# Optimization experiments

Hardware: AMD Instinct MI355X
Metric: run time of the kernel (lower is better)

## Reference

```python
import jax, jax.numpy as jnp
import numpy as np
from jax import lax

SMOOTH = 1.0
CONVEX = 1.0
MAX_IT = 500  # eval=False path in legendre
TOL = 0.001
B, C, H = 1024, 64, 128


def _icnn(x, Wy0, by0, Wy1, by1, Wz1, Wy2, by2, Wz2):
    # ICNN: softplus chain with positive (clamped) Wz weights, plus strongly-convex quadratic term
    h = jax.nn.softplus(x @ Wy0.T + by0)                                   # [B, H]
    h = jax.nn.softplus(h @ jnp.clip(Wz1, 0.0, 1e10).T + x @ Wy1.T + by1)  # [B, H]
    out = jax.nn.softplus(h @ jnp.clip(Wz2, 0.0, 1e10).T + x @ Wy2.T + by2)  # [B, 1]
    return out + (1.0 / (2.0 * SMOOTH)) * jnp.sum(x * x, axis=1, keepdims=True)


def _legendre(z, Wy0, by0, Wy1, by1, Wz1, Wy2, by2, Wz2):
    # grad of per-sample scalar ICNN output w.r.t. its input (sum trick: outputs are sample-wise independent)
    grad_icnn = jax.grad(lambda xx: jnp.sum(_icnn(xx, Wy0, by0, Wy1, by1, Wz1, Wy2, by2, Wz2)))
    step = 2.0 * SMOOTH

    def body(carry, i):
        x1, done = carry
        g = grad_icnn(x1)
        new_x1 = x1 + (step / (i + 1.0)) * (z - g)
        x1 = jnp.where(done, x1, new_x1)
        err = jnp.mean(jnp.linalg.norm(z - g, axis=1))
        done = jnp.logical_or(done, err < TOL)
        return (x1, done), None

    x1_0 = jnp.ones_like(z)
    (x1, _), _ = lax.scan(body, (x1_0, jnp.array(False)), jnp.arange(MAX_IT, dtype=z.dtype))
    return x1 + CONVEX * z


def _xavier(key, shape):
    fan_out, fan_in = shape
    std = np.sqrt(2.0 / (fan_in + fan_out))
    return jax.random.normal(key, shape, dtype=jnp.float32) * std


def setup_inputs() -> dict:
    key = jax.random.key(0)
    ks = jax.random.split(key, 8)
    bound0 = 1.0 / np.sqrt(C)
    return {
        "x": jax.random.normal(ks[0], (B, C), dtype=jnp.float32),
        "Wy0": _xavier(ks[1], (H, C)),
        "by0": jax.random.uniform(ks[2], (H,), dtype=jnp.float32, minval=-bound0, maxval=bound0),
        "Wy1": _xavier(ks[3], (H, C)),
        "by1": jax.random.uniform(ks[4], (H,), dtype=jnp.float32, minval=-bound0, maxval=bound0),
        "Wz1": _xavier(ks[5], (H, H)),
        "Wy2": _xavier(ks[6], (1, C)),
        "by2": jax.random.uniform(ks[7], (1,), dtype=jnp.float32, minval=-bound0, maxval=bound0),
        "Wz2": _xavier(jax.random.fold_in(key, 99), (1, H)),
    }


def reference(x, Wy0, by0, Wy1, by1, Wz1, Wy2, by2, Wz2):
    return _legendre(x, Wy0, by0, Wy1, by1, Wz1, Wy2, by2, Wz2)
```

## Files before the change

kernel.cpp:

```cpp
#include <hip/hip_runtime.h>
#include <math.h>

#define NB 1024
#define NC 64
#define NH 128
#define MAX_IT 500
#define TOLF 1e-3f

typedef _Float16 f16x8 __attribute__((ext_vector_type(8)));
typedef float    f32x4 __attribute__((ext_vector_type(4)));
typedef _Float16 h2    __attribute__((ext_vector_type(2)));

#define MFMA(a, b, c) __builtin_amdgcn_mfma_f32_16x16x32_f16((a), (b), (c), 0, 0, 0)

__device__ __forceinline__ unsigned pack_h2(float a, float b) {
    union { h2 h; unsigned u; } cv;
    cv.h.x = (_Float16)a; cv.h.y = (_Float16)b; return cv.u;
}
__device__ __forceinline__ float rcp_fast(float x) {
#if __has_builtin(__builtin_amdgcn_rcpf)
    return __builtin_amdgcn_rcpf(x);
#else
    return 1.0f / x;
#endif
}
__device__ __forceinline__ void sigsp(float a, float& sig, float& sp) {
    const float e = __expf(-fabsf(a));
    const float r = rcp_fast(1.0f + e);
    sig = (a >= 0.0f) ? r : e * r;
    sp  = fmaxf(a, 0.0f) + __logf(1.0f + e);
}
__device__ __forceinline__ float sigm(float a) {
    const float e = __expf(-fabsf(a));
    const float r = rcp_fast(1.0f + e);
    return (a >= 0.0f) ? r : e * r;
}
__device__ __forceinline__ float clp(float x) { return fmaxf(x, 0.0f); }

__launch_bounds__(256, 1)
__global__ void blnn_kernel(const float* __restrict__ xin,
                            const float* __restrict__ Wy0,
                            const float* __restrict__ by0,
                            const float* __restrict__ Wy1,
                            const float* __restrict__ by1,
                            const float* __restrict__ Wz1,
                            const float* __restrict__ Wy2,
                            const float* __restrict__ by2,
                            const float* __restrict__ Wz2,
                            float* __restrict__ out)
{
    __shared__ uint4 WA0q[16 * 64];
    __shared__ uint4 WA1q[16 * 64];
    __shared__ uint4 WAZq[32 * 64];
    __shared__ uint4 WZTq[32 * 64];
    __shared__ uint4 W1Tq[16 * 64];
    __shared__ uint4 W0Tq[16 * 64];
    __shared__ __align__(16) _Float16 xact [4 * 72];
    __shared__ __align__(16) _Float16 h0act[4 * 136];
    __shared__ __align__(16) _Float16 v1act[4 * 136];
    __shared__ __align__(16) _Float16 v0act[4 * 136];
    __shared__ __align__(16) float by0f[128], by1f[128], wz2f[128];
    __shared__ __align__(16) float hp[16], pxp[16], npar[16];

    const int tid  = threadIdx.x;
    const int w    = tid >> 6;
    const int l    = tid & 63;
    const int n    = l & 15;
    const int n4   = n & 3;
    const int quad = l >> 4;
    const int blk4 = blockIdx.x * 4;

    for (int f = tid; f < 16 * 64; f += 256) {
        const int tile = f >> 6, q = f & 63;
        const int mt = tile >> 1, ks = tile & 1;
        const int row = mt * 16 + (q & 15);
        const int k0  = ks * 32 + ((q >> 4) << 3);
        const float* p0 = Wy0 + row * 64 + k0;
        WA0q[f] = make_uint4(pack_h2(p0[0], p0[1]), pack_h2(p0[2], p0[3]),
                             pack_h2(p0[4], p0[5]), pack_h2(p0[6], p0[7]));
        const float* p1 = Wy1 + row * 64 + k0;
        WA1q[f] = make_uint4(pack_h2(p1[0], p1[1]), pack_h2(p1[2], p1[3]),
                             pack_h2(p1[4], p1[5]), pack_h2(p1[6], p1[7]));
    }
    for (int f = tid; f < 32 * 64; f += 256) {
        const int tile = f >> 6, q = f & 63;
        const int mt = tile >> 2, ks = tile & 3;
        const int row = mt * 16 + (q & 15);
        const int k0  = ks * 32 + ((q >> 4) << 3);
        const float* p = Wz1 + row * 128 + k0;
        WAZq[f] = make_uint4(pack_h2(clp(p[0]), clp(p[1])), pack_h2(clp(p[2]), clp(p[3])),
                             pack_h2(clp(p[4]), clp(p[5])), pack_h2(clp(p[6]), clp(p[7])));
        const float* pt = Wz1 + k0 * 128 + row;
        WZTq[f] = make_uint4(pack_h2(clp(pt[0]),   clp(pt[128])),
                             pack_h2(clp(pt[256]), clp(pt[384])),
                             pack_h2(clp(pt[512]), clp(pt[640])),
                             pack_h2(clp(pt[768]), clp(pt[896])));
    }
    for (int f = tid; f < 16 * 64; f += 256) {
        const int tile = f >> 6, q = f & 63;
        const int mt = tile >> 2, ks = tile & 3;
        const int rowT = mt * 16 + (q & 15);
        const int k0   = ks * 32 + ((q >> 4) << 3);
        const float* p1 = Wy1 + k0 * 64 + rowT;
        W1Tq[f] = make_uint4(pack_h2(p1[0],   p1[64]),  pack_h2(p1[128], p1[192]),
                             pack_h2(p1[256], p1[320]), pack_h2(p1[384], p1[448]));
        const float* p0 = Wy0 + k0 * 64 + rowT;
        W0Tq[f] = make_uint4(pack_h2(p0[0],   p0[64]),  pack_h2(p0[128], p0[192]),
                             pack_h2(p0[256], p0[320]), pack_h2(p0[384], p0[448]));
    }
    if (tid < 128) {
        by0f[tid] = by0[tid];
        by1f[tid] = by1[tid];
        wz2f[tid] = fmaxf(Wz2[tid], 0.0f);
    }
    {
        const int nn = tid >> 6, cc = tid & 63;
        xact[nn * 72 + cc] = (_Float16)xin[(blk4 + nn) * 64 + cc];
    }

    const float4 z4  = ((const float4*)xin)[(blk4 + n4) * 16 + w * 4 + quad];
    const float4 wy4 = ((const float4*)Wy2)[w * 4 + quad];
    float zr[4]   = {z4.x, z4.y, z4.z, z4.w};
    float wy2r[4] = {wy4.x, wy4.y, wy4.z, wy4.w};
    float xcur[4] = {zr[0], zr[1], zr[2], zr[3]};
    float lamE = 1.0f, prevn2 = 3.4e38f;
    const float b2 = by2[0];

    {
        float pxs = wy2r[0]*xcur[0] + wy2r[1]*xcur[1] + wy2r[2]*xcur[2] + wy2r[3]*xcur[3];
        pxs += __shfl_xor(pxs, 16, 64);
        pxs += __shfl_xor(pxs, 32, 64);
        if (l < 4) pxp[l * 4 + w] = pxs;
    }
    __syncthreads();

    const f16x8* WA0v = (const f16x8*)WA0q;
    const f16x8* WA1v = (const f16x8*)WA1q;
    const f16x8* WAZv = (const f16x8*)WAZq;
    const f16x8* WZTv = (const f16x8*)WZTq;
    const f16x8* W1Tv = (const f16x8*)W1Tq;
    const f16x8* W0Tv = (const f16x8*)W0Tq;
    const float4* by0v = (const float4*)by0f;
    const float4* by1v = (const float4*)by1f;
    const float4* wz2v = (const float4*)wz2f;
    const _Float16* xrow  = xact  + n4 * 72;
    const _Float16* h0row = h0act + n4 * 136;
    const _Float16* v1row = v1act + n4 * 136;
    const _Float16* v0row = v0act + n4 * 136;

    float sig0[2][4];

    for (int it = 0; it < MAX_IT; ++it) {
        f16x8 bx0 = *(const f16x8*)(xrow + quad * 8);
        f16x8 bx1 = *(const f16x8*)(xrow + 32 + quad * 8);
        #pragma unroll
        for (int mi = 0; mi < 2; ++mi) {
            const int mt = w + 4 * mi;
            f32x4 acc = {0.f, 0.f, 0.f, 0.f};
            acc = MFMA(WA0v[(mt * 2 + 0) * 64 + l], bx0, acc);
            acc = MFMA(WA0v[(mt * 2 + 1) * 64 + l], bx1, acc);
            const float4 bb = by0v[mt * 4 + quad];
            float sp0, sp1, sp2, sp3;
            sigsp(acc[0] + bb.x, sig0[mi][0], sp0);
            sigsp(acc[1] + bb.y, sig0[mi][1], sp1);
            sigsp(acc[2] + bb.z, sig0[mi][2], sp2);
            sigsp(acc[3] + bb.w, sig0[mi][3], sp3);
            if (n < 4)
                *(uint2*)&h0act[n4 * 136 + mt * 16 + quad * 4] =
                    make_uint2(pack_h2(sp0, sp1), pack_h2(sp2, sp3));
        }
        __syncthreads();

        f16x8 bh0 = *(const f16x8*)(h0row + quad * 8);
        f16x8 bh1 = *(const f16x8*)(h0row + 32 + quad * 8);
        f16x8 bh2 = *(const f16x8*)(h0row + 64 + quad * 8);
        f16x8 bh3 = *(const f16x8*)(h0row + 96 + quad * 8);
        float hsum = 0.0f;
        #pragma unroll
        for (int mi = 0; mi < 2; ++mi) {
            const int mt = w + 4 * mi;
            f32x4 acc = {0.f, 0.f, 0.f, 0.f};
            acc = MFMA(WAZv[(mt * 4 + 0) * 64 + l], bh0, acc);
            acc = MFMA(WAZv[(mt * 4 + 1) * 64 + l], bh1, acc);
            acc = MFMA(WAZv[(mt * 4 + 2) * 64 + l], bh2, acc);
            acc = MFMA(WAZv[(mt * 4 + 3) * 64 + l], bh3, acc);
            acc = MFMA(WA1v[(mt * 2 + 0) * 64 + l], bx0, acc);
            acc = MFMA(WA1v[(mt * 2 + 1) * 64 + l], bx1, acc);
            const float4 bb  = by1v[mt * 4 + quad];
            const float4 wzq = wz2v[mt * 4 + quad];
            float s1, h1;
            sigsp(acc[0] + bb.x, s1, h1); hsum = fmaf(wzq.x, h1, hsum);
            const float t0 = s1 * wzq.x;
            sigsp(acc[1] + bb.y, s1, h1); hsum = fmaf(wzq.y, h1, hsum);
            const float t1 = s1 * wzq.y;
            sigsp(acc[2] + bb.z, s1, h1); hsum = fmaf(wzq.z, h1, hsum);
            const float t2 = s1 * wzq.z;
            sigsp(acc[3] + bb.w, s1, h1); hsum = fmaf(wzq.w, h1, hsum);
            const float t3 = s1 * wzq.w;
            if (n < 4)
                *(uint2*)&v1act[n4 * 136 + mt * 16 + quad * 4] =
                    make_uint2(pack_h2(t0, t1), pack_h2(t2, t3));
        }
        hsum += __shfl_xor(hsum, 16, 64);
        hsum += __shfl_xor(hsum, 32, 64);
        if (l < 4) hp[l * 4 + w] = hsum;
        __syncthreads();

        float sg2c;
        {
            const float4 hv = ((const float4*)hp)[n4];
            const float4 pv = ((const float4*)pxp)[n4];
            sg2c = sigm(hv.x + hv.y + hv.z + hv.w + pv.x + pv.y + pv.z + pv.w + b2);
        }
        f16x8 bv10 = *(const f16x8*)(v1row + quad * 8);
        f16x8 bv11 = *(const f16x8*)(v1row + 32 + quad * 8);
        f16x8 bv12 = *(const f16x8*)(v1row + 64 + quad * 8);
        f16x8 bv13 = *(const f16x8*)(v1row + 96 + quad * 8);
        #pragma unroll
        for (int mi = 0; mi < 2; ++mi) {
            const int mt = w + 4 * mi;
            f32x4 acc = {0.f, 0.f, 0.f, 0.f};
            acc = MFMA(WZTv[(mt * 4 + 0) * 64 + l], bv10, acc);
            acc = MFMA(WZTv[(mt * 4 + 1) * 64 + l], bv11, acc);
            acc = MFMA(WZTv[(mt * 4 + 2) * 64 + l], bv12, acc);
            acc = MFMA(WZTv[(mt * 4 + 3) * 64 + l], bv13, acc);
            const float a0 = sig0[mi][0] * sg2c * acc[0];
            const float a1 = sig0[mi][1] * sg2c * acc[1];
            const float a2 = sig0[mi][2] * sg2c * acc[2];
            const float a3 = sig0[mi][3] * sg2c * acc[3];
            if (n < 4)
                *(uint2*)&v0act[n4 * 136 + mt * 16 + quad * 4] =
                    make_uint2(pack_h2(a0, a1), pack_h2(a2, a3));
        }
        f32x4 accg = {0.f, 0.f, 0.f, 0.f};
        accg = MFMA(W1Tv[(w * 4 + 0) * 64 + l], bv10, accg);
        accg = MFMA(W1Tv[(w * 4 + 1) * 64 + l], bv11, accg);
        accg = MFMA(W1Tv[(w * 4 + 2) * 64 + l], bv12, accg);
        accg = MFMA(W1Tv[(w * 4 + 3) * 64 + l], bv13, accg);
        __syncthreads();

        f16x8 bv00 = *(const f16x8*)(v0row + quad * 8);
        f16x8 bv01 = *(const f16x8*)(v0row + 32 + quad * 8);
        f16x8 bv02 = *(const f16x8*)(v0row + 64 + quad * 8);
        f16x8 bv03 = *(const f16x8*)(v0row + 96 + quad * 8);
        f32x4 acc0 = {0.f, 0.f, 0.f, 0.f};
        acc0 = MFMA(W0Tv[(w * 4 + 0) * 64 + l], bv00, acc0);
        acc0 = MFMA(W0Tv[(w * 4 + 1) * 64 + l], bv01, acc0);
        acc0 = MFMA(W0Tv[(w * 4 + 2) * 64 + l], bv02, acc0);
        acc0 = MFMA(W0Tv[(w * 4 + 3) * 64 + l], bv03, acc0);
        float resid[4];
        float r2 = 0.0f;
        #pragma unroll
        for (int r = 0; r < 4; ++r) {
            const float g = xcur[r] + sg2c * wy2r[r] + sg2c * accg[r] + acc0[r];
            resid[r] = zr[r] - g;
            r2 = fmaf(resid[r], resid[r], r2);
        }
        r2 += __shfl_xor(r2, 16, 64);
        r2 += __shfl_xor(r2, 32, 64);
        if (l < 4) npar[l * 4 + w] = r2;
        __syncthreads();

        const float4 q0 = ((const float4*)npar)[0];
        const float4 q1 = ((const float4*)npar)[1];
        const float4 q2 = ((const float4*)npar)[2];
        const float4 q3 = ((const float4*)npar)[3];
        const float s0 = q0.x + q0.y + q0.z + q0.w;
        const float s1 = q1.x + q1.y + q1.z + q1.w;
        const float s2 = q2.x + q2.y + q2.z + q2.w;
        const float s3 = q3.x + q3.y + q3.z + q3.w;
        const float T2 = TOLF * TOLF;
        if (s0 < T2 && s1 < T2 && s2 < T2 && s3 < T2) break;

        const float myn2 = (n4 == 0) ? s0 : (n4 == 1) ? s1 : (n4 == 2) ? s2 : s3;
        if (myn2 >= T2) {
            if (myn2 > prevn2 * 0.998f)      lamE *= 0.5f;
            else if (myn2 < 0.81f * prevn2)  lamE = fminf(lamE * 1.15f, 1.0f);
            const float step = fmaxf(lamE, 1.0f / (float)(it + 2));
            #pragma unroll
            for (int r = 0; r < 4; ++r) xcur[r] = fmaf(step, resid[r], xcur[r]);
            prevn2 = myn2;
        }
        {
            float pxs = wy2r[0]*xcur[0] + wy2r[1]*xcur[1] + wy2r[2]*xcur[2] + wy2r[3]*xcur[3];
            pxs += __shfl_xor(pxs, 16, 64);
            pxs += __shfl_xor(pxs, 32, 64);
            if (l < 4) pxp[l * 4 + w] = pxs;
        }
        if (n < 4)
            *(uint2*)&xact[n4 * 72 + w * 16 + quad * 4] =
                make_uint2(pack_h2(xcur[0], xcur[1]), pack_h2(xcur[2], xcur[3]));
        __syncthreads();
    }

    if (n < 4) {
        float4 o;
        o.x = xcur[0] + zr[0]; o.y = xcur[1] + zr[1];
        o.z = xcur[2] + zr[2]; o.w = xcur[3] + zr[3];
        ((float4*)out)[(blk4 + n4) * 16 + w * 4 + quad] = o;
    }
}

extern "C" void kernel_launch(void* const* d_in, const int* in_sizes, int n_in,
                              void* d_out, int out_size, void* d_ws, size_t ws_size,
                              hipStream_t stream) {
    const float* xin = (const float*)d_in[0];
    const float* Wy0 = (const float*)d_in[1];
    const float* by0 = (const float*)d_in[2];
    const float* Wy1 = (const float*)d_in[3];
    const float* by1 = (const float*)d_in[4];
    const float* Wz1 = (const float*)d_in[5];
    const float* Wy2 = (const float*)d_in[6];
    const float* by2 = (const float*)d_in[7];
    const float* Wz2 = (const float*)d_in[8];
    float* out = (float*)d_out;

    blnn_kernel<<<dim3(NB / 4), dim3(256), 0, stream>>>(
        xin, Wy0, by0, Wy1, by1, Wz1, Wy2, by2, Wz2, out);
}
```

Measured before the change: 88.29 us.

## Halve samples per block, hold adjoint weights in registers, prepack via separate kernel

Each block now handles 2 samples instead of 4, so the grid doubles to 512 blocks and launch bounds allow 2 blocks per CU. The transposed weights used in the backward pass (Wz1^T, Wy1^T, Wy0^T) are packed to fp16 once by a new pre-kernel into workspace and then loaded into registers instead of LDS, which cuts LDS use and per-iteration LDS reads. The step-size rule also drops the increase branch for lamE, which changes the convergence behaviour and possibly the iteration count. Register pressure goes up, and with only 2 samples per 16-column MFMA tile most of the tensor-core work is wasted padding.

```diff
diff --git a/kernel.cpp b/kernel.cpp
--- a/kernel.cpp
+++ b/kernel.cpp
@@ -2,8 +2,6 @@
 #include <math.h>
 
 #define NB 1024
-#define NC 64
-#define NH 128
 #define MAX_IT 500
 #define TOLF 1e-3f
 
@@ -16,6 +14,9 @@
 __device__ __forceinline__ unsigned pack_h2(float a, float b) {
     union { h2 h; unsigned u; } cv;
     cv.h.x = (_Float16)a; cv.h.y = (_Float16)b; return cv.u;
+}
+__device__ __forceinline__ f16x8 as_f16x8(uint4 u) {
+    union { uint4 u; f16x8 h; } cv; cv.u = u; return cv.h;
 }
 __device__ __forceinline__ float rcp_fast(float x) {
 #if __has_builtin(__builtin_amdgcn_rcpf)
@@ -37,7 +38,44 @@
 }
 __device__ __forceinline__ float clp(float x) { return fmaxf(x, 0.0f); }
 
-__launch_bounds__(256, 1)
+__global__ void pack_adj(const float* __restrict__ Wy0,
+                         const float* __restrict__ Wy1,
+                         const float* __restrict__ Wz1,
+                         uint4* __restrict__ ws)
+{
+    const int f = blockIdx.x * 256 + threadIdx.x;
+    if (f < 2048) {
+        const int tile = f >> 6, q = f & 63;
+        const int mt = tile >> 2, ks = tile & 3;
+        const int row = mt * 16 + (q & 15);
+        const int k0  = ks * 32 + ((q >> 4) << 3);
+        const float* pt = Wz1 + k0 * 128 + row;
+        ws[f] = make_uint4(pack_h2(clp(pt[0]),   clp(pt[128])),
+                           pack_h2(clp(pt[256]), clp(pt[384])),
+                           pack_h2(clp(pt[512]), clp(pt[640])),
+                           pack_h2(clp(pt[768]), clp(pt[896])));
+    } else if (f < 3072) {
+        const int f2 = f - 2048;
+        const int tile = f2 >> 6, q = f2 & 63;
+        const int mt = tile >> 2, ks = tile & 3;
+        const int rowT = mt * 16 + (q & 15);
+        const int k0   = ks * 32 + ((q >> 4) << 3);
+        const float* p = Wy1 + k0 * 64 + rowT;
+        ws[f] = make_uint4(pack_h2(p[0],   p[64]),  pack_h2(p[128], p[192]),
+                           pack_h2(p[256], p[320]), pack_h2(p[384], p[448]));
+    } else {
+        const int f2 = f - 3072;
+        const int tile = f2 >> 6, q = f2 & 63;
+        const int mt = tile >> 2, ks = tile & 3;
+        const int rowT = mt * 16 + (q & 15);
+        const int k0   = ks * 32 + ((q >> 4) << 3);
+        const float* p = Wy0 + k0 * 64 + rowT;
+        ws[f] = make_uint4(pack_h2(p[0],   p[64]),  pack_h2(p[128], p[192]),
+                           pack_h2(p[256], p[320]), pack_h2(p[384], p[448]));
+    }
+}
+
+__launch_bounds__(256, 2)
 __global__ void blnn_kernel(const float* __restrict__ xin,
                             const float* __restrict__ Wy0,
                             const float* __restrict__ by0,
@@ -47,28 +85,26 @@
                             const float* __restrict__ Wy2,
                             const float* __restrict__ by2,
                             const float* __restrict__ Wz2,
+                            const uint4* __restrict__ adjw,
                             float* __restrict__ out)
 {
     __shared__ uint4 WA0q[16 * 64];
     __shared__ uint4 WA1q[16 * 64];
     __shared__ uint4 WAZq[32 * 64];
-    __shared__ uint4 WZTq[32 * 64];
-    __shared__ uint4 W1Tq[16 * 64];
-    __shared__ uint4 W0Tq[16 * 64];
-    __shared__ __align__(16) _Float16 xact [4 * 72];
-    __shared__ __align__(16) _Float16 h0act[4 * 136];
-    __shared__ __align__(16) _Float16 v1act[4 * 136];
-    __shared__ __align__(16) _Float16 v0act[4 * 136];
+    __shared__ __align__(16) _Float16 xact [2 * 72];
+    __shared__ __align__(16) _Float16 h0act[2 * 136];
+    __shared__ __align__(16) _Float16 v1act[2 * 136];
+    __shared__ __align__(16) _Float16 v0act[2 * 136];
     __shared__ __align__(16) float by0f[128], by1f[128], wz2f[128];
-    __shared__ __align__(16) float hp[16], pxp[16], npar[16];
+    __shared__ __align__(16) float hp[8], pxp[8], npar[8];
 
     const int tid  = threadIdx.x;
     const int w    = tid >> 6;
     const int l    = tid & 63;
     const int n    = l & 15;
-    const int n4   = n & 3;
+    const int n2   = n & 1;
     const int quad = l >> 4;
-    const int blk4 = blockIdx.x * 4;
+    const int blk2 = blockIdx.x * 2;
 
     for (int f = tid; f < 16 * 64; f += 256) {
         const int tile = f >> 6, q = f & 63;
@@ -90,35 +126,38 @@
         const float* p = Wz1 + row * 128 + k0;
         WAZq[f] = make_uint4(pack_h2(clp(p[0]), clp(p[1])), pack_h2(clp(p[2]), clp(p[3])),
                              pack_h2(clp(p[4]), clp(p[5])), pack_h2(clp(p[6]), clp(p[7])));
-        const float* pt = Wz1 + k0 * 128 + row;
-        WZTq[f] = make_uint4(pack_h2(clp(pt[0]),   clp(pt[128])),
-                             pack_h2(clp(pt[256]), clp(pt[384])),
-                             pack_h2(clp(pt[512]), clp(pt[640])),
-                             pack_h2(clp(pt[768]), clp(pt[896])));
-    }
-    for (int f = tid; f < 16 * 64; f += 256) {
-        const int tile = f >> 6, q = f & 63;
-        const int mt = tile >> 2, ks = tile & 3;
-        const int rowT = mt * 16 + (q & 15);
-        const int k0   = ks * 32 + ((q >> 4) << 3);
-        const float* p1 = Wy1 + k0 * 64 + rowT;
-        W1Tq[f] = make_uint4(pack_h2(p1[0],   p1[64]),  pack_h2(p1[128], p1[192]),
-                             pack_h2(p1[256], p1[320]), pack_h2(p1[384], p1[448]));
-        const float* p0 = Wy0 + k0 * 64 + rowT;
-        W0Tq[f] = make_uint4(pack_h2(p0[0],   p0[64]),  pack_h2(p0[128], p0[192]),
-                             pack_h2(p0[256], p0[320]), pack_h2(p0[384], p0[448]));
     }
     if (tid < 128) {
         by0f[tid] = by0[tid];
         by1f[tid] = by1[tid];
         wz2f[tid] = fmaxf(Wz2[tid], 0.0f);
     }
-    {
+    if (tid < 128) {
         const int nn = tid >> 6, cc = tid & 63;
-        xact[nn * 72 + cc] = (_Float16)xin[(blk4 + nn) * 64 + cc];
-    }
-
-    const float4 z4  = ((const float4*)xin)[(blk4 + n4) * 16 + w * 4 + quad];
+        xact[nn * 72 + cc] = (_Float16)xin[(blk2 + nn) * 64 + cc];
+    }
+
+    const uint4* WZTg = adjw;
+    const uint4* W1Tg = adjw + 2048;
+    const uint4* W0Tg = adjw + 3072;
+    const uint4 rz0 = WZTg[((w    ) * 4 + 0) * 64 + l];
+    const uint4 rz1 = WZTg[((w    ) * 4 + 1) * 64 + l];
+    const uint4 rz2 = WZTg[((w    ) * 4 + 2) * 64 + l];
+    const uint4 rz3 = WZTg[((w    ) * 4 + 3) * 64 + l];
+    const uint4 rz4 = WZTg[((w + 4) * 4 + 0) * 64 + l];
+    const uint4 rz5 = WZTg[((w + 4) * 4 + 1) * 64 + l];
+    const uint4 rz6 = WZTg[((w + 4) * 4 + 2) * 64 + l];
+    const uint4 rz7 = WZTg[((w + 4) * 4 + 3) * 64 + l];
+    const uint4 r1_0 = W1Tg[(w * 4 + 0) * 64 + l];
+    const uint4 r1_1 = W1Tg[(w * 4 + 1) * 64 + l];
+    const uint4 r1_2 = W1Tg[(w * 4 + 2) * 64 + l];
+    const uint4 r1_3 = W1Tg[(w * 4 + 3) * 64 + l];
+    const uint4 r0_0 = W0Tg[(w * 4 + 0) * 64 + l];
+    const uint4 r0_1 = W0Tg[(w * 4 + 1) * 64 + l];
+    const uint4 r0_2 = W0Tg[(w * 4 + 2) * 64 + l];
+    const uint4 r0_3 = W0Tg[(w * 4 + 3) * 64 + l];
+
+    const float4 z4  = ((const float4*)xin)[(blk2 + n2) * 16 + w * 4 + quad];
     const float4 wy4 = ((const float4*)Wy2)[w * 4 + quad];
     float zr[4]   = {z4.x, z4.y, z4.z, z4.w};
     float wy2r[4] = {wy4.x, wy4.y, wy4.z, wy4.w};
@@ -130,23 +169,20 @@
         float pxs = wy2r[0]*xcur[0] + wy2r[1]*xcur[1] + wy2r[2]*xcur[2] + wy2r[3]*xcur[3];
         pxs += __shfl_xor(pxs, 16, 64);
         pxs += __shfl_xor(pxs, 32, 64);
-        if (l < 4) pxp[l * 4 + w] = pxs;
+        if (l < 2) pxp[l * 4 + w] = pxs;
     }
     __syncthreads();
 
     const f16x8* WA0v = (const f16x8*)WA0q;
     const f16x8* WA1v = (const f16x8*)WA1q;
     const f16x8* WAZv = (const f16x8*)WAZq;
-    const f16x8* WZTv = (const f16x8*)WZTq;
-    const f16x8* W1Tv = (const f16x8*)W1Tq;
-    const f16x8* W0Tv = (const f16x8*)W0Tq;
     const float4* by0v = (const float4*)by0f;
     const float4* by1v = (const float4*)by1f;
     const float4* wz2v = (const float4*)wz2f;
-    const _Float16* xrow  = xact  + n4 * 72;
-    const _Float16* h0row = h0act + n4 * 136;
-    const _Float16* v1row = v1act + n4 * 136;
-    const _Float16* v0row = v0act + n4 * 136;
+    const _Float16* xrow  = xact  + n2 * 72;
+    const _Float16* h0row = h0act + n2 * 136;
+    const _Float16* v1row = v1act + n2 * 136;
+    const _Float16* v0row = v0act + n2 * 136;
 
     float sig0[2][4];
 
@@ -165,8 +201,8 @@
             sigsp(acc[1] + bb.y, sig0[mi][1], sp1);
             sigsp(acc[2] + bb.z, sig0[mi][2], sp2);
             sigsp(acc[3] + bb.w, sig0[mi][3], sp3);
-            if (n < 4)
-                *(uint2*)&h0act[n4 * 136 + mt * 16 + quad * 4] =
+            if (n < 2)
+                *(uint2*)&h0act[n2 * 136 + mt * 16 + quad * 4] =
                     make_uint2(pack_h2(sp0, sp1), pack_h2(sp2, sp3));
         }
         __syncthreads();
@@ -197,46 +233,58 @@
             const float t2 = s1 * wzq.z;
             sigsp(acc[3] + bb.w, s1, h1); hsum = fmaf(wzq.w, h1, hsum);
             const float t3 = s1 * wzq.w;
-            if (n < 4)
-                *(uint2*)&v1act[n4 * 136 + mt * 16 + quad * 4] =
+            if (n < 2)
+                *(uint2*)&v1act[n2 * 136 + mt * 16 + quad * 4] =
                     make_uint2(pack_h2(t0, t1), pack_h2(t2, t3));
         }
         hsum += __shfl_xor(hsum, 16, 64);
         hsum += __shfl_xor(hsum, 32, 64);
-        if (l < 4) hp[l * 4 + w] = hsum;
+        if (l < 2) hp[l * 4 + w] = hsum;
         __syncthreads();
 
         float sg2c;
         {
-            const float4 hv = ((const float4*)hp)[n4];
-            const float4 pv = ((const float4*)pxp)[n4];
+            const float4 hv = ((const float4*)hp)[n2];
+            const float4 pv = ((const float4*)pxp)[n2];
             sg2c = sigm(hv.x + hv.y + hv.z + hv.w + pv.x + pv.y + pv.z + pv.w + b2);
         }
         f16x8 bv10 = *(const f16x8*)(v1row + quad * 8);
         f16x8 bv11 = *(const f16x8*)(v1row + 32 + quad * 8);
         f16x8 bv12 = *(const f16x8*)(v1row + 64 + quad * 8);
         f16x8 bv13 = *(const f16x8*)(v1row + 96 + quad * 8);
-        #pragma unroll
-        for (int mi = 0; mi < 2; ++mi) {
-            const int mt = w + 4 * mi;
+        {
             f32x4 acc = {0.f, 0.f, 0.f, 0.f};
-            acc = MFMA(WZTv[(mt * 4 + 0) * 64 + l], bv10, acc);
-            acc = MFMA(WZTv[(mt * 4 + 1) * 64 + l], bv11, acc);
-            acc = MFMA(WZTv[(mt * 4 + 2) * 64 + l], bv12, acc);
-            acc = MFMA(WZTv[(mt * 4 + 3) * 64 + l], bv13, acc);
-            const float a0 = sig0[mi][0] * sg2c * acc[0];
-            const float a1 = sig0[mi][1] * sg2c * acc[1];
-            const float a2 = sig0[mi][2] * sg2c * acc[2];
-            const float a3 = sig0[mi][3] * sg2c * acc[3];
-            if (n < 4)
-                *(uint2*)&v0act[n4 * 136 + mt * 16 + quad * 4] =
+            acc = MFMA(as_f16x8(rz0), bv10, acc);
+            acc = MFMA(as_f16x8(rz1), bv11, acc);
+            acc = MFMA(as_f16x8(rz2), bv12, acc);
+            acc = MFMA(as_f16x8(rz3), bv13, acc);
+            const float a0 = sig0[0][0] * sg2c * acc[0];
+            const float a1 = sig0[0][1] * sg2c * acc[1];
+            const float a2 = sig0[0][2] * sg2c * acc[2];
+            const float a3 = sig0[0][3] * sg2c * acc[3];
+            if (n < 2)
+                *(uint2*)&v0act[n2 * 136 + w * 16 + quad * 4] =
                     make_uint2(pack_h2(a0, a1), pack_h2(a2, a3));
         }
+        {
+            f32x4 acc = {0.f, 0.f, 0.f, 0.f};
+            acc = MFMA(as_f16x8(rz4), bv10, acc);
+            acc = MFMA(as_f16x8(rz5), bv11, acc);
+            acc = MFMA(as_f16x8(rz6), bv12, acc);
+            acc = MFMA(as_f16x8(rz7), bv13, acc);
+            const float a0 = sig0[1][0] * sg2c * acc[0];
+            const float a1 = sig0[1][1] * sg2c * acc[1];
+            const float a2 = sig0[1][2] * sg2c * acc[2];
+            const float a3 = sig0[1][3] * sg2c * acc[3];
+            if (n < 2)
+                *(uint2*)&v0act[n2 * 136 + (w + 4) * 16 + quad * 4] =
+                    make_uint2(pack_h2(a0, a1), pack_h2(a2, a3));
+        }
         f32x4 accg = {0.f, 0.f, 0.f, 0.f};
-        accg = MFMA(W1Tv[(w * 4 + 0) * 64 + l], bv10, accg);
-        accg = MFMA(W1Tv[(w * 4 + 1) * 64 + l], bv11, accg);
-        accg = MFMA(W1Tv[(w * 4 + 2) * 64 + l], bv12, accg);
-        accg = MFMA(W1Tv[(w * 4 + 3) * 64 + l], bv13, accg);
+        accg = MFMA(as_f16x8(r1_0), bv10, accg);
+        accg = MFMA(as_f16x8(r1_1), bv11, accg);
+        accg = MFMA(as_f16x8(r1_2), bv12, accg);
+        accg = MFMA(as_f16x8(r1_3), bv13, accg);
         __syncthreads();
 
         f16x8 bv00 = *(const f16x8*)(v0row + quad * 8);
@@ -244,10 +292,10 @@
         f16x8 bv02 = *(const f16x8*)(v0row + 64 + quad * 8);
         f16x8 bv03 = *(const f16x8*)(v0row + 96 + quad * 8);
         f32x4 acc0 = {0.f, 0.f, 0.f, 0.f};
-        acc0 = MFMA(W0Tv[(w * 4 + 0) * 64 + l], bv00, acc0);
-        acc0 = MFMA(W0Tv[(w * 4 + 1) * 64 + l], bv01, acc0);
-        acc0 = MFMA(W0Tv[(w * 4 + 2) * 64 + l], bv02, acc0);
-        acc0 = MFMA(W0Tv[(w * 4 + 3) * 64 + l], bv03, acc0);
+        acc0 = MFMA(as_f16x8(r0_0), bv00, acc0);
+        acc0 = MFMA(as_f16x8(r0_1), bv01, acc0);
+        acc0 = MFMA(as_f16x8(r0_2), bv02, acc0);
+        acc0 = MFMA(as_f16x8(r0_3), bv03, acc0);
         float resid[4];
         float r2 = 0.0f;
         #pragma unroll
@@ -258,24 +306,19 @@
         }
         r2 += __shfl_xor(r2, 16, 64);
         r2 += __shfl_xor(r2, 32, 64);
-        if (l < 4) npar[l * 4 + w] = r2;
+        if (l < 2) npar[l * 4 + w] = r2;
         __syncthreads();
 
         const float4 q0 = ((const float4*)npar)[0];
         const float4 q1 = ((const float4*)npar)[1];
-        const float4 q2 = ((const float4*)npar)[2];
-        const float4 q3 = ((const float4*)npar)[3];
         const float s0 = q0.x + q0.y + q0.z + q0.w;
         const float s1 = q1.x + q1.y + q1.z + q1.w;
-        const float s2 = q2.x + q2.y + q2.z + q2.w;
-        const float s3 = q3.x + q3.y + q3.z + q3.w;
         const float T2 = TOLF * TOLF;
-        if (s0 < T2 && s1 < T2 && s2 < T2 && s3 < T2) break;
-
-        const float myn2 = (n4 == 0) ? s0 : (n4 == 1) ? s1 : (n4 == 2) ? s2 : s3;
+        if (s0 < T2 && s1 < T2) break;
+
+        const float myn2 = n2 ? s1 : s0;
         if (myn2 >= T2) {
-            if (myn2 > prevn2 * 0.998f)      lamE *= 0.5f;
-            else if (myn2 < 0.81f * prevn2)  lamE = fminf(lamE * 1.15f, 1.0f);
+            if (myn2 > prevn2 * 0.998f) lamE *= 0.5f;
             const float step = fmaxf(lamE, 1.0f / (float)(it + 2));
             #pragma unroll
             for (int r = 0; r < 4; ++r) xcur[r] = fmaf(step, resid[r], xcur[r]);
@@ -285,19 +328,19 @@
             float pxs = wy2r[0]*xcur[0] + wy2r[1]*xcur[1] + wy2r[2]*xcur[2] + wy2r[3]*xcur[3];
             pxs += __shfl_xor(pxs, 16, 64);
             pxs += __shfl_xor(pxs, 32, 64);
-            if (l < 4) pxp[l * 4 + w] = pxs;
-        }
-        if (n < 4)
-            *(uint2*)&xact[n4 * 72 + w * 16 + quad * 4] =
+            if (l < 2) pxp[l * 4 + w] = pxs;
+        }
+        if (n < 2)
+            *(uint2*)&xact[n2 * 72 + w * 16 + quad * 4] =
                 make_uint2(pack_h2(xcur[0], xcur[1]), pack_h2(xcur[2], xcur[3]));
         __syncthreads();
     }
 
-    if (n < 4) {
+    if (n < 2) {
         float4 o;
         o.x = xcur[0] + zr[0]; o.y = xcur[1] + zr[1];
         o.z = xcur[2] + zr[2]; o.w = xcur[3] + zr[3];
-        ((float4*)out)[(blk4 + n4) * 16 + w * 4 + quad] = o;
+        ((float4*)out)[(blk2 + n2) * 16 + w * 4 + quad] = o;
     }
 }
 
@@ -315,6 +358,8 @@
     const float* Wz2 = (const float*)d_in[8];
     float* out = (float*)d_out;
 
-    blnn_kernel<<<dim3(NB / 4), dim3(256), 0, stream>>>(
-        xin, Wy0, by0, Wy1, by1, Wz1, Wy2, by2, Wz2, out);
-}
+    pack_adj<<<dim3(16), dim3(256), 0, stream>>>(Wy0, Wy1, Wz1, (uint4*)d_ws);
+    blnn_kernel<<<dim3(NB / 2), dim3(256), 0, stream>>>(
+        xin, Wy0, by0, Wy1, by1, Wz1, Wy2, by2, Wz2,
+        (const uint4*)d_ws, out);
+}
```

After: 93.62 us. +6.0%, slower.
